# Performance work log

Hardware: AMD Instinct MI355X
Metric: run time of the kernel (lower is better)

## Reference

```python
import jax, jax.numpy as jnp
import numpy as np

EPS = 1e-5
NUM_GROUPS = 32


def group_norm(x, scale, bias):
    # x: [B, C, H, W], 32 groups, normalized over (C/G, H, W)
    B, C, H, W = x.shape
    G = NUM_GROUPS
    xg = x.reshape(B, G, C // G, H, W)
    mean = xg.mean(axis=(2, 3, 4), keepdims=True)
    var = xg.var(axis=(2, 3, 4), keepdims=True)
    xg = (xg - mean) * jax.lax.rsqrt(var + EPS)
    x = xg.reshape(B, C, H, W)
    return x * scale[None, :, None, None] + bias[None, :, None, None]


def setup_inputs() -> dict:
    key = jax.random.key(0)
    ks = jax.random.split(key, 6)
    B, C, H, W = 32, 512, 32, 32
    std = 1.0 / np.sqrt(C)
    return {
        "x": jax.random.normal(ks[0], (B, C, H, W), dtype=jnp.float32),
        "gn_scale": jnp.ones((C,), dtype=jnp.float32),
        "gn_bias": jnp.zeros((C,), dtype=jnp.float32),
        "wq": jax.random.normal(ks[1], (C, C), dtype=jnp.float32) * std,
        "bq": jnp.zeros((C,), dtype=jnp.float32),
        "wk": jax.random.normal(ks[2], (C, C), dtype=jnp.float32) * std,
        "bk": jnp.zeros((C,), dtype=jnp.float32),
        "wv": jax.random.normal(ks[3], (C, C), dtype=jnp.float32) * std,
        "bv": jnp.zeros((C,), dtype=jnp.float32),
        "wo": jax.random.normal(ks[4], (C, C), dtype=jnp.float32) * std,
        "bo": jnp.zeros((C,), dtype=jnp.float32),
    }


def reference(x, gn_scale, gn_bias, wq, bq, wk, bk, wv, bv, wo, bo):
    B, C, H, W = x.shape
    h = group_norm(x, gn_scale, gn_bias)
    # 1x1 convs == per-pixel matmuls; flatten spatial to tokens: [B, HW, C]
    ht = h.reshape(B, C, H * W).transpose(0, 2, 1)
    q = jnp.einsum('bnc,oc->bno', ht, wq) + bq  # [B, HW, C]
    k = jnp.einsum('bnc,oc->bno', ht, wk) + bk
    v = jnp.einsum('bnc,oc->bno', ht, wv) + bv
    scale = 1.0 / jnp.sqrt(jnp.asarray(C, x.dtype))
    w = jnp.einsum('bnc,bmc->bnm', q, k) * scale  # [B, HW, HW]
    w = jax.nn.softmax(w, axis=-1)
    a = jnp.einsum('bnm,bmc->bnc', w, v)  # [B, HW, C]
    out = jnp.einsum('bnc,oc->bno', a, wo) + bo
    out = out.transpose(0, 2, 1).reshape(B, C, H, W)
    return x + out
```

## Files before the change

kernel.cpp:

```cpp
#include <hip/hip_runtime.h>
#include <stdint.h>

typedef unsigned short u16;
typedef __attribute__((ext_vector_type(8))) short short8;
typedef __attribute__((ext_vector_type(4))) short s16x4;
typedef __attribute__((ext_vector_type(4))) float f32x4;

#define NTOK 1024
#define CDIM 512
#define NG 32

#define GLOAD_LDS16(gptr, lptr)                                                              \
  __builtin_amdgcn_global_load_lds((const __attribute__((address_space(1))) unsigned int*)(gptr), \
                                   (__attribute__((address_space(3))) unsigned int*)(lptr), 16, 0, 0)

__device__ __forceinline__ u16 f2bf(float f) {
  union { float f; uint32_t u; } v; v.f = f;
  uint32_t r = v.u + 0x7fffu + ((v.u >> 16) & 1u);
  return (u16)(r >> 16);
}

__device__ __forceinline__ float bf2f(u16 b) {
  union { uint32_t u; float f; } v; v.u = ((uint32_t)b) << 16;
  return v.f;
}

__global__ __launch_bounds__(256) void wconv(const float* __restrict__ wq, const float* __restrict__ wk,
                                             const float* __restrict__ wv, const float* __restrict__ wo,
                                             const float* __restrict__ bq, const float* __restrict__ bk,
                                             const float* __restrict__ bv,
                                             u16* __restrict__ out, float* __restrict__ bqkv) {
  int i = blockIdx.x * 256 + threadIdx.x;
  out[i]          = f2bf(wq[i]);
  out[262144 + i] = f2bf(wk[i]);
  out[524288 + i] = f2bf(wv[i]);
  out[786432 + i] = f2bf(wo[i]);
  if (i < 512) bqkv[i] = bq[i];
  else if (i < 1024) bqkv[i] = bk[i - 512];
  else if (i < 1536) bqkv[i] = bv[i - 1024];
}

__global__ __launch_bounds__(256) void gn_stats(const float* __restrict__ x,
                                                float* __restrict__ mean_o, float* __restrict__ rstd_o) {
  int bg = blockIdx.x;
  const float4* base = (const float4*)(x + (size_t)bg * 16384);
  float s = 0.f, ss = 0.f;
  for (int i = threadIdx.x; i < 4096; i += 256) {
    float4 v = base[i];
    s  += v.x + v.y + v.z + v.w;
    ss += v.x * v.x + v.y * v.y + v.z * v.z + v.w * v.w;
  }
#pragma unroll
  for (int d = 1; d < 64; d <<= 1) { s += __shfl_xor(s, d); ss += __shfl_xor(ss, d); }
  __shared__ float as[4], as2[4];
  int w = threadIdx.x >> 6;
  if ((threadIdx.x & 63) == 0) { as[w] = s; as2[w] = ss; }
  __syncthreads();
  if (threadIdx.x == 0) {
    float S = as[0] + as[1] + as[2] + as[3];
    float SS = as2[0] + as2[1] + as2[2] + as2[3];
    float m = S * (1.f / 16384.f);
    float var = SS * (1.f / 16384.f) - m * m;
    mean_o[bg] = m;
    rstd_o[bg] = rsqrtf(var + 1e-5f);
  }
}

__global__ __launch_bounds__(256) void gn_apply(const float* __restrict__ x,
                                                const float* __restrict__ mean_, const float* __restrict__ rstd_,
                                                const float* __restrict__ gsc, const float* __restrict__ gbi,
                                                u16* __restrict__ h) {
  int n0 = blockIdx.x * 64, c0 = blockIdx.y * 64, b = blockIdx.z;
  __shared__ u16 t[64][65];
  int tid = threadIdx.x;
  int nl4 = (tid & 15) * 4;
  int clb = tid >> 4;
#pragma unroll
  for (int p = 0; p < 4; ++p) {
    int cl = p * 16 + clb;
    int c = c0 + cl;
    int g = c >> 4;
    float m = mean_[b * NG + g], rs = rstd_[b * NG + g];
    float sc = gsc[c] * rs, bi = gbi[c] - m * sc;
    float4 v = *(const float4*)(x + ((size_t)b * CDIM + c) * NTOK + n0 + nl4);
    t[cl][nl4 + 0] = f2bf(v.x * sc + bi);
    t[cl][nl4 + 1] = f2bf(v.y * sc + bi);
    t[cl][nl4 + 2] = f2bf(v.z * sc + bi);
    t[cl][nl4 + 3] = f2bf(v.w * sc + bi);
  }
  __syncthreads();
  int nl = tid >> 3;
  int cc = (tid & 7) * 8;
#pragma unroll
  for (int p = 0; p < 2; ++p) {
    int n = nl + p * 32;
    short8 o;
#pragma unroll
    for (int i = 0; i < 8; ++i) o[i] = (short)t[cc + i][n];
    *(short8*)(h + (size_t)(b * NTOK + n0 + n) * CDIM + c0 + cc) = o;
  }
}

template <int MODE>
__device__ __forceinline__ void gemm_body(const u16* __restrict__ A, const u16* __restrict__ B,
                                          const float* __restrict__ bias, u16* __restrict__ outb,
                                          u16* __restrict__ outb2,
                                          float* __restrict__ outf, const float* __restrict__ resid,
                                          int Ka, int Kb, int nkt,
                                          size_t strideA, size_t strideB, int batch0) {
  int nx = gridDim.x, ny = gridDim.y;
  int nwg = nx * ny * gridDim.z;
  int id = blockIdx.x + nx * (blockIdx.y + ny * blockIdx.z);
  int cpx = nwg >> 3;
  int sw = (id & 7) * cpx + (id >> 3);
  int bx = sw % nx; int t_ = sw / nx;
  int by = t_ % ny; int z = t_ / ny;

  const u16* Amat = A + (size_t)z * strideA;
  const u16* Bmat = B + (size_t)z * strideB;
  int n0 = bx * 256, m0 = by * 256;
  __shared__ __align__(16) u16 SH[65536];
  int tid = threadIdx.x;
  int l = tid & 63, wid = tid >> 6;
  int lr = l & 15, lh = l >> 4;
  int wm = (wid >> 2) * 128;
  int wn = (wid & 3) * 64;

  f32x4 acc[8][4];
#pragma unroll
  for (int i = 0; i < 8; ++i)
#pragma unroll
    for (int j = 0; j < 4; ++j) acc[i][j] = (f32x4){0.f, 0.f, 0.f, 0.f};

  short8 af[4][2];
  short8 bf01[2][2];
  short8 bf23[2][2];

  int sr = tid >> 3, sc = tid & 7;
  int sg = (sc ^ (sr & 7)) << 3;
  const u16* Ag0 = Amat + (size_t)(m0 + sr) * Ka + sg;
  const u16* Ag1 = Ag0 + (size_t)64 * Ka;
  const u16* Bg0 = Bmat + (size_t)(n0 + sr) * Kb + sg;
  const u16* Bg1 = Bg0 + (size_t)64 * Kb;
  size_t hA = (size_t)128 * Ka, hB = (size_t)128 * Kb;
  u16* Al0 = SH + sr * 64 + sc * 8;
  u16* Bl0 = SH + 32768 + sr * 64 + sc * 8;

#define STAGE_A(bufsel, ktv, half)                                        \
  {                                                                       \
    size_t go_ = (size_t)(ktv) * 64 + ((half) ? hA : (size_t)0);          \
    u16* ld_ = Al0 + (bufsel) * 16384 + (half) * 8192;                    \
    GLOAD_LDS16(Ag0 + go_, ld_);                                          \
    GLOAD_LDS16(Ag1 + go_, ld_ + 4096);                                   \
  }
#define STAGE_B(bufsel, ktv, half)                                        \
  {                                                                       \
    size_t go_ = (size_t)(ktv) * 64 + ((half) ? hB : (size_t)0);          \
    u16* ld_ = Bl0 + (bufsel) * 16384 + (half) * 8192;                    \
    GLOAD_LDS16(Bg0 + go_, ld_);                                          \
    GLOAD_LDS16(Bg1 + go_, ld_ + 4096);                                   \
  }

#define READ_AF(ihalf, bufsel)                                                        \
  _Pragma("unroll") for (int i_ = 0; i_ < 4; ++i_) {                                  \
    int row_ = wm + (ihalf) * 64 + i_ * 16 + lr;                                      \
    const u16* p_ = SH + (bufsel) * 16384 + row_ * 64;                                \
    _Pragma("unroll") for (int ks_ = 0; ks_ < 2; ++ks_)                               \
      af[i_][ks_] = *(const short8*)(p_ + (((ks_ * 4 + lh) ^ (row_ & 7)) << 3));      \
  }

#define READ_BF(dst, jbase, bufsel)                                                   \
  _Pragma("unroll") for (int j_ = 0; j_ < 2; ++j_) {                                  \
    int row_ = wn + ((jbase) + j_) * 16 + lr;                                         \
    const u16* p_ = SH + 32768 + (bufsel) * 16384 + row_ * 64;                        \
    _Pragma("unroll") for (int ks_ = 0; ks_ < 2; ++ks_)                               \
      dst[j_][ks_] = *(const short8*)(p_ + (((ks_ * 4 + lh) ^ (row_ & 7)) << 3));     \
  }

#define MFMA_Q(ihalf, jbase, bsrc)                                                    \
  _Pragma("unroll") for (int ks_ = 0; ks_ < 2; ++ks_)                                 \
    _Pragma("unroll") for (int i_ = 0; i_ < 4; ++i_)                                  \
      _Pragma("unroll") for (int j_ = 0; j_ < 2; ++j_)                                \
        acc[(ihalf) * 4 + i_][(jbase) + j_] = __builtin_amdgcn_mfma_f32_16x16x32_bf16( \
            af[i_][ks_], bsrc[j_][ks_], acc[(ihalf) * 4 + i_][(jbase) + j_], 0, 0, 0);

#define PBAR() __builtin_amdgcn_s_barrier()

#define PHASES(BC, BN, GI, DOHI, DOLO)                                    \
  {                                                                       \
    int g1_ = (GI) + 1, g2_ = (GI) + 2;                                   \
                                           \
    READ_AF(0, BC);                                                       \
    READ_BF(bf01, 0, BC);                                                 \
    if (DOHI) { STAGE_A(BN, g1_, 1); }                                    \
    PBAR();                                                               \
    __builtin_amdgcn_s_setprio(1);                                        \
    MFMA_Q(0, 0, bf01);                                                   \
    __builtin_amdgcn_s_setprio(0);                                        \
    PBAR();                                                               \
                                           \
    READ_BF(bf23, 2, BC);                                                 \
    if (DOHI) { STAGE_B(BN, g1_, 1); }                                    \
    PBAR();                                                               \
    __builtin_amdgcn_s_setprio(1);                                        \
    MFMA_Q(0, 2, bf23);                                                   \
    __builtin_amdgcn_s_setprio(0);                                        \
    PBAR();                                                               \
     \
    READ_AF(1, BC);                                                       \
    if (DOLO) { STAGE_B(BC, g2_, 0); }                                    \
    PBAR();                                                               \
    __builtin_amdgcn_s_setprio(1);                                        \
    MFMA_Q(1, 2, bf23);                                                   \
    __builtin_amdgcn_s_setprio(0);                                        \
    PBAR();                                                               \
     \
    if (DOLO) { STAGE_A(BC, g2_, 0); }                                    \
    PBAR();                                                               \
    __builtin_amdgcn_s_setprio(1);                                        \
    MFMA_Q(1, 0, bf01);                                                   \
    __builtin_amdgcn_s_setprio(0);                                        \
    if (DOLO) { asm volatile("s_waitcnt vmcnt(4)"); }                     \
    else      { asm volatile("s_waitcnt vmcnt(0)"); }                     \
    __builtin_amdgcn_sched_barrier(0);                                    \
    PBAR();                                                               \
  }

  int k1 = (1 < nkt) ? 1 : 0;
  STAGE_B(0, 0, 0);
  STAGE_A(0, 0, 0);
  STAGE_A(0, 0, 1);
  STAGE_B(0, 0, 1);
  STAGE_B(1, k1, 0);
  STAGE_A(1, k1, 0);
  asm volatile("s_waitcnt vmcnt(4)");
  __builtin_amdgcn_sched_barrier(0);
  PBAR();

  for (int kt = 0; kt < nkt; kt += 2) {
    int more = (kt + 2 < nkt) ? 1 : 0;
    PHASES(0, 1, kt, 1, more);
    PHASES(1, 0, kt + 1, more, more);
  }

  __syncthreads();
  const int gr0 = m0 + wm, gc0 = n0 + wn;
  u16* eb = SH + wid * 4352;

  if constexpr (MODE == 5) {
    float bj[4];
#pragma unroll
    for (int j = 0; j < 4; ++j) bj[j] = bias[gc0 + j * 16 + lr];
    if (n0 < 1024) {
#pragma unroll
      for (int pass = 0; pass < 2; ++pass) {
#pragma unroll
        for (int i2 = 0; i2 < 4; ++i2)
#pragma unroll
          for (int j = 0; j < 4; ++j)
#pragma unroll
            for (int r = 0; r < 4; ++r)
              eb[(i2 * 16 + lh * 4 + r) * 68 + j * 16 + lr] =
                  f2bf(acc[pass * 4 + i2][j][r] + bj[j]);
        asm volatile("s_waitcnt lgkmcnt(0)");
        __builtin_amdgcn_sched_barrier(0);
#pragma unroll
        for (int t = 0; t < 8; ++t) {
          int row = t * 8 + (l >> 3), c8 = (l & 7) * 8;
          s16x4 lo = *(const s16x4*)(eb + row * 68 + c8);
          s16x4 hi = *(const s16x4*)(eb + row * 68 + c8 + 4);
          short8 o;
          o[0] = lo[0]; o[1] = lo[1]; o[2] = lo[2]; o[3] = lo[3];
          o[4] = hi[0]; o[5] = hi[1]; o[6] = hi[2]; o[7] = hi[3];
          *(short8*)(outb + (size_t)(gr0 + pass * 64 + row) * 1024 + gc0 + c8) = o;
        }
        asm volatile("s_waitcnt lgkmcnt(0)");
        __builtin_amdgcn_sched_barrier(0);
      }
    } else {
      int ch0 = gc0 - 1024;
      int bt = m0 >> 10, tok0 = (m0 & 1023) + wm;
#pragma unroll
      for (int pass = 0; pass < 2; ++pass) {
#pragma unroll
        for (int i2 = 0; i2 < 4; ++i2)
#pragma unroll
          for (int j = 0; j < 4; ++j) {
            s16x4 w;
#pragma unroll
            for (int r = 0; r < 4; ++r)
              w[r] = (short)f2bf(acc[pass * 4 + i2][j][r] + bj[j]);
            *(s16x4*)(eb + (j * 16 + lr) * 68 + i2 * 16 + lh * 4) = w;
          }
        asm volatile("s_waitcnt lgkmcnt(0)");
        __builtin_amdgcn_sched_barrier(0);
#pragma unroll
        for (int t = 0; t < 8; ++t) {
          int row = t * 8 + (l >> 3), c8 = (l & 7) * 8;
          s16x4 lo = *(const s16x4*)(eb + row * 68 + c8);
          s16x4 hi = *(const s16x4*)(eb + row * 68 + c8 + 4);
          short8 o;
          o[0] = lo[0]; o[1] = lo[1]; o[2] = lo[2]; o[3] = lo[3];
          o[4] = hi[0]; o[5] = hi[1]; o[6] = hi[2]; o[7] = hi[3];
          *(short8*)(outb2 + (size_t)(bt * 512 + ch0 + row) * 1024 + tok0 + pass * 64 + c8) = o;
        }
        asm volatile("s_waitcnt lgkmcnt(0)");
        __builtin_amdgcn_sched_barrier(0);
      }
    }
  } else if constexpr (MODE == 3 || MODE == 4) {
    u16* obase = (MODE == 3) ? (outb + (size_t)z * 1048576)
                             : (outb + (size_t)(batch0 + z) * 524288);
    const int LD = (MODE == 3) ? 1024 : 512;
#pragma unroll
    for (int pass = 0; pass < 2; ++pass) {
#pragma unroll
      for (int i2 = 0; i2 < 4; ++i2)
#pragma unroll
        for (int j = 0; j < 4; ++j)
#pragma unroll
          for (int r = 0; r < 4; ++r)
            eb[(i2 * 16 + lh * 4 + r) * 68 + j * 16 + lr] =
                f2bf(acc[pass * 4 + i2][j][r]);
      asm volatile("s_waitcnt lgkmcnt(0)");
      __builtin_amdgcn_sched_barrier(0);
#pragma unroll
      for (int t = 0; t < 8; ++t) {
        int row = t * 8 + (l >> 3), c8 = (l & 7) * 8;
        s16x4 lo = *(const s16x4*)(eb + row * 68 + c8);
        s16x4 hi = *(const s16x4*)(eb + row * 68 + c8 + 4);
        short8 o;
        o[0] = lo[0]; o[1] = lo[1]; o[2] = lo[2]; o[3] = lo[3];
        o[4] = hi[0]; o[5] = hi[1]; o[6] = hi[2]; o[7] = hi[3];
        *(short8*)(obase + (size_t)(gr0 + pass * 64 + row) * LD + gc0 + c8) = o;
      }
      asm volatile("s_waitcnt lgkmcnt(0)");
      __builtin_amdgcn_sched_barrier(0);
    }
  } else {
    float* ebf = (float*)SH + wid * 2176;
    int bt = n0 >> 10, nn0 = (n0 & 1023) + wn;
#pragma unroll
    for (int pass = 0; pass < 4; ++pass) {
#pragma unroll
      for (int i2 = 0; i2 < 2; ++i2)
#pragma unroll
        for (int r = 0; r < 4; ++r) {
          float bv = bias[gr0 + pass * 32 + i2 * 16 + lh * 4 + r];
#pragma unroll
          for (int j = 0; j < 4; ++j)
            ebf[(i2 * 16 + lh * 4 + r) * 68 + j * 16 + lr] =
                acc[pass * 2 + i2][j][r] + bv;
        }
      asm volatile("s_waitcnt lgkmcnt(0)");
      __builtin_amdgcn_sched_barrier(0);
#pragma unroll
      for (int t = 0; t < 8; ++t) {
        int row = t * 4 + (l >> 4), c4 = (l & 15) * 4;
        float4 vv = *(const float4*)(ebf + row * 68 + c4);
        size_t addr = ((size_t)bt * 512 + gr0 + pass * 32 + row) * 1024 + nn0 + c4;
        const float4 rr = *(const float4*)(resid + addr);
        vv.x += rr.x; vv.y += rr.y; vv.z += rr.z; vv.w += rr.w;
        *(float4*)(outf + addr) = vv;
      }
      asm volatile("s_waitcnt lgkmcnt(0)");
      __builtin_amdgcn_sched_barrier(0);
    }
  }
#undef STAGE_A
#undef STAGE_B
#undef READ_AF
#undef READ_BF
#undef MFMA_Q
#undef PBAR
#undef PHASES
}

__global__ __launch_bounds__(512, 2) void gemm_qkv(const u16* A, const u16* B, const float* bias,
                                                   u16* outb, u16* outb2, float* outf, const float* resid,
                                                   int Ka, int Kb, int nkt, size_t sA, size_t sB, int b0) {
  gemm_body<5>(A, B, bias, outb, outb2, outf, resid, Ka, Kb, nkt, sA, sB, b0);
}
__global__ __launch_bounds__(512, 2) void gemm_o(const u16* A, const u16* B, const float* bias,
                                                 u16* outb, u16* outb2, float* outf, const float* resid,
                                                 int Ka, int Kb, int nkt, size_t sA, size_t sB, int b0) {
  gemm_body<2>(A, B, bias, outb, outb2, outf, resid, Ka, Kb, nkt, sA, sB, b0);
}
__global__ __launch_bounds__(512, 2) void gemm_s(const u16* A, const u16* B, const float* bias,
                                                 u16* outb, u16* outb2, float* outf, const float* resid,
                                                 int Ka, int Kb, int nkt, size_t sA, size_t sB, int b0) {
  gemm_body<3>(A, B, bias, outb, outb2, outf, resid, Ka, Kb, nkt, sA, sB, b0);
}
__global__ __launch_bounds__(512, 2) void gemm_pv(const u16* A, const u16* B, const float* bias,
                                                  u16* outb, u16* outb2, float* outf, const float* resid,
                                                  int Ka, int Kb, int nkt, size_t sA, size_t sB, int b0) {
  gemm_body<4>(A, B, bias, outb, outb2, outf, resid, Ka, Kb, nkt, sA, sB, b0);
}

__global__ __launch_bounds__(256) void softmax_rows(u16* __restrict__ S) {
  const float scale = 0.04419417382415922f;
  int row = blockIdx.x * 4 + (threadIdx.x >> 6);
  int l = threadIdx.x & 63;
  u16* Sr = S + (size_t)row * 1024;
  short8 a = *(const short8*)(Sr + l * 8);
  short8 b = *(const short8*)(Sr + 512 + l * 8);
  float f[16];
#pragma unroll
  for (int i = 0; i < 8; ++i) { f[i] = bf2f((u16)a[i]); f[8 + i] = bf2f((u16)b[i]); }
  float mx = f[0];
#pragma unroll
  for (int i = 1; i < 16; ++i) mx = fmaxf(mx, f[i]);
#pragma unroll
  for (int d = 1; d < 64; d <<= 1) mx = fmaxf(mx, __shfl_xor(mx, d));
  float s = 0.f;
#pragma unroll
  for (int i = 0; i < 16; ++i) { f[i] = __expf((f[i] - mx) * scale); s += f[i]; }
#pragma unroll
  for (int d = 1; d < 64; d <<= 1) s += __shfl_xor(s, d);
  float inv = 1.f / s;
  short8 oa, ob;
#pragma unroll
  for (int i = 0; i < 8; ++i) { oa[i] = (short)f2bf(f[i] * inv); ob[i] = (short)f2bf(f[8 + i] * inv); }
  *(short8*)(Sr + l * 8) = oa;
  *(short8*)(Sr + 512 + l * 8) = ob;
}

extern "C" void kernel_launch(void* const* d_in, const int* in_sizes, int n_in,
                              void* d_out, int out_size, void* d_ws, size_t ws_size,
                              hipStream_t stream) {
  const float* x   = (const float*)d_in[0];
  const float* gsc = (const float*)d_in[1];
  const float* gbi = (const float*)d_in[2];
  const float* wq  = (const float*)d_in[3];
  const float* bq  = (const float*)d_in[4];
  const float* wk  = (const float*)d_in[5];
  const float* bk  = (const float*)d_in[6];
  const float* wv  = (const float*)d_in[7];
  const float* bv  = (const float*)d_in[8];
  const float* wo  = (const float*)d_in[9];
  const float* bo  = (const float*)d_in[10];

  char* ws = (char*)d_ws;
  u16* wbf = (u16*)ws;
  float* bqkv = (float*)(ws + (2ull << 20));
  float* mean_ = (float*)(ws + (2ull << 20) + 65536);
  float* rstd_ = mean_ + 1024;
  u16* h   = (u16*)(ws + (4ull << 20));
  u16* qk  = (u16*)(ws + (36ull << 20));
  u16* vm  = (u16*)(ws + (100ull << 20));
  u16* S   = (u16*)(ws + (132ull << 20));
  u16* am  = h;
  float* out = (float*)d_out;

  size_t sbytes = ws_size > (132ull << 20) ? ws_size - (132ull << 20) : 0;
  int CB = 1;
  while (CB < 32 && (size_t)(CB * 2) * (2ull << 20) <= sbytes) CB *= 2;

  wconv<<<1024, 256, 0, stream>>>(wq, wk, wv, wo, bq, bk, bv, wbf, bqkv);
  gn_stats<<<1024, 256, 0, stream>>>(x, mean_, rstd_);
  gn_apply<<<dim3(16, 8, 32), 256, 0, stream>>>(x, mean_, rstd_, gsc, gbi, h);
  gemm_qkv<<<dim3(6, 128), 512, 0, stream>>>(h, wbf, bqkv, qk, vm, nullptr, nullptr,
                                             512, 512, 8, 0, 0, 0);
  for (int c0 = 0; c0 < 32; c0 += CB) {
    gemm_s<<<dim3(4, 4, CB), 512, 0, stream>>>(qk + (size_t)c0 * 1048576, qk + 512 + (size_t)c0 * 1048576,
                                               nullptr, S, nullptr, nullptr, nullptr,
                                               1024, 1024, 8, 1048576, 1048576, 0);
    softmax_rows<<<CB * 256, 256, 0, stream>>>(S);
    gemm_pv<<<dim3(2, 4, CB), 512, 0, stream>>>(S, vm + (size_t)c0 * 524288,
                                                nullptr, am, nullptr, nullptr, nullptr,
                                                1024, 1024, 16, 1048576, 524288, c0);
  }
  gemm_o<<<dim3(128, 2), 512, 0, stream>>>(wbf + 786432, am, bo, nullptr, nullptr, out, x,
                                           512, 512, 8, 0, 0, 0);
}
```

Before: 241.8 us.

## Fuse softmax into score GEMM epilogue and PV GEMM row-sum normalization

Drops the separate softmax kernel. The score GEMM epilogue now writes exp(score*scale) directly in bf16. The PV GEMM sums each row of its A fragments (the exp values) while loading them, reduces those sums across lanes, keeps them in LDS, and divides the output rows by them in a new MODE 4 epilogue. This removes a full read and write pass over the 1024x1024 score matrix per batch. The cost is extra ALU work inside the PV main loop, and dropping the max-subtraction step risks overflow if scores grow large.

```diff
diff --git a/kernel.cpp b/kernel.cpp
--- a/kernel.cpp
+++ b/kernel.cpp
@@ -132,6 +132,10 @@
 #pragma unroll
     for (int j = 0; j < 4; ++j) acc[i][j] = (f32x4){0.f, 0.f, 0.f, 0.f};
 
+  float rs[8];
+#pragma unroll
+  for (int i = 0; i < 8; ++i) rs[i] = 0.f;
+
   short8 af[4][2];
   short8 bf01[2][2];
   short8 bf23[2][2];
@@ -169,6 +173,14 @@
       af[i_][ks_] = *(const short8*)(p_ + (((ks_ * 4 + lh) ^ (row_ & 7)) << 3));      \
   }
 
+#define SUM_AF(ihalf)                                                                 \
+  if (MODE == 4) {                                                                    \
+    _Pragma("unroll") for (int i_ = 0; i_ < 4; ++i_)                                  \
+      _Pragma("unroll") for (int ks_ = 0; ks_ < 2; ++ks_)                             \
+        _Pragma("unroll") for (int e_ = 0; e_ < 8; ++e_)                              \
+          rs[(ihalf) * 4 + i_] += bf2f((u16)af[i_][ks_][e_]);                         \
+  }
+
 #define READ_BF(dst, jbase, bufsel)                                                   \
   _Pragma("unroll") for (int j_ = 0; j_ < 2; ++j_) {                                  \
     int row_ = wn + ((jbase) + j_) * 16 + lr;                                         \
@@ -191,6 +203,7 @@
     int g1_ = (GI) + 1, g2_ = (GI) + 2;                                   \
                                            \
     READ_AF(0, BC);                                                       \
+    SUM_AF(0);                                                            \
     READ_BF(bf01, 0, BC);                                                 \
     if (DOHI) { STAGE_A(BN, g1_, 1); }                                    \
     PBAR();                                                               \
@@ -208,6 +221,7 @@
     PBAR();                                                               \
      \
     READ_AF(1, BC);                                                       \
+    SUM_AF(1);                                                            \
     if (DOLO) { STAGE_B(BC, g2_, 0); }                                    \
     PBAR();                                                               \
     __builtin_amdgcn_s_setprio(1);                                        \
@@ -241,6 +255,20 @@
     int more = (kt + 2 < nkt) ? 1 : 0;
     PHASES(0, 1, kt, 1, more);
     PHASES(1, 0, kt + 1, more, more);
+  }
+
+  if (MODE == 4) {
+#pragma unroll
+    for (int p = 0; p < 8; ++p) {
+      rs[p] += __shfl_xor(rs[p], 16);
+      rs[p] += __shfl_xor(rs[p], 32);
+    }
+    if (lh == 0) {
+      float* rsum_ = (float*)(SH + 64512);
+#pragma unroll
+      for (int p = 0; p < 8; ++p)
+        rsum_[wm + (p >> 2) * 64 + (p & 3) * 16 + lr] = rs[p];
+    }
   }
 
   __syncthreads();
@@ -308,10 +336,9 @@
         __builtin_amdgcn_sched_barrier(0);
       }
     }
-  } else if constexpr (MODE == 3 || MODE == 4) {
-    u16* obase = (MODE == 3) ? (outb + (size_t)z * 1048576)
-                             : (outb + (size_t)(batch0 + z) * 524288);
-    const int LD = (MODE == 3) ? 1024 : 512;
+  } else if constexpr (MODE == 3) {
+    const float scale = 0.04419417382415922f;
+    u16* obase = outb + (size_t)z * 1048576;
 #pragma unroll
     for (int pass = 0; pass < 2; ++pass) {
 #pragma unroll
@@ -321,7 +348,7 @@
 #pragma unroll
           for (int r = 0; r < 4; ++r)
             eb[(i2 * 16 + lh * 4 + r) * 68 + j * 16 + lr] =
-                f2bf(acc[pass * 4 + i2][j][r]);
+                f2bf(__expf(acc[pass * 4 + i2][j][r] * scale));
       asm volatile("s_waitcnt lgkmcnt(0)");
       __builtin_amdgcn_sched_barrier(0);
 #pragma unroll
@@ -332,7 +359,37 @@
         short8 o;
         o[0] = lo[0]; o[1] = lo[1]; o[2] = lo[2]; o[3] = lo[3];
         o[4] = hi[0]; o[5] = hi[1]; o[6] = hi[2]; o[7] = hi[3];
-        *(short8*)(obase + (size_t)(gr0 + pass * 64 + row) * LD + gc0 + c8) = o;
+        *(short8*)(obase + (size_t)(gr0 + pass * 64 + row) * 1024 + gc0 + c8) = o;
+      }
+      asm volatile("s_waitcnt lgkmcnt(0)");
+      __builtin_amdgcn_sched_barrier(0);
+    }
+  } else if constexpr (MODE == 4) {
+    const float* rsum_ = (const float*)(SH + 64512);
+    u16* obase = outb + (size_t)(batch0 + z) * 524288;
+#pragma unroll
+    for (int pass = 0; pass < 2; ++pass) {
+#pragma unroll
+      for (int i2 = 0; i2 < 4; ++i2)
+#pragma unroll
+        for (int r = 0; r < 4; ++r) {
+          float inv_ = 1.f / rsum_[wm + pass * 64 + i2 * 16 + lh * 4 + r];
+#pragma unroll
+          for (int j = 0; j < 4; ++j)
+            eb[(i2 * 16 + lh * 4 + r) * 68 + j * 16 + lr] =
+                f2bf(acc[pass * 4 + i2][j][r] * inv_);
+        }
+      asm volatile("s_waitcnt lgkmcnt(0)");
+      __builtin_amdgcn_sched_barrier(0);
+#pragma unroll
+      for (int t = 0; t < 8; ++t) {
+        int row = t * 8 + (l >> 3), c8 = (l & 7) * 8;
+        s16x4 lo = *(const s16x4*)(eb + row * 68 + c8);
+        s16x4 hi = *(const s16x4*)(eb + row * 68 + c8 + 4);
+        short8 o;
+        o[0] = lo[0]; o[1] = lo[1]; o[2] = lo[2]; o[3] = lo[3];
+        o[4] = hi[0]; o[5] = hi[1]; o[6] = hi[2]; o[7] = hi[3];
+        *(short8*)(obase + (size_t)(gr0 + pass * 64 + row) * 512 + gc0 + c8) = o;
       }
       asm volatile("s_waitcnt lgkmcnt(0)");
       __builtin_amdgcn_sched_barrier(0);
@@ -370,6 +427,7 @@
 #undef STAGE_A
 #undef STAGE_B
 #undef READ_AF
+#undef SUM_AF
 #undef READ_BF
 #undef MFMA_Q
 #undef PBAR
@@ -395,34 +453,6 @@
                                                   u16* outb, u16* outb2, float* outf, const float* resid,
                                                   int Ka, int Kb, int nkt, size_t sA, size_t sB, int b0) {
   gemm_body<4>(A, B, bias, outb, outb2, outf, resid, Ka, Kb, nkt, sA, sB, b0);
-}
-
-__global__ __launch_bounds__(256) void softmax_rows(u16* __restrict__ S) {
-  const float scale = 0.04419417382415922f;
-  int row = blockIdx.x * 4 + (threadIdx.x >> 6);
-  int l = threadIdx.x & 63;
-  u16* Sr = S + (size_t)row * 1024;
-  short8 a = *(const short8*)(Sr + l * 8);
-  short8 b = *(const short8*)(Sr + 512 + l * 8);
-  float f[16];
-#pragma unroll
-  for (int i = 0; i < 8; ++i) { f[i] = bf2f((u16)a[i]); f[8 + i] = bf2f((u16)b[i]); }
-  float mx = f[0];
-#pragma unroll
-  for (int i = 1; i < 16; ++i) mx = fmaxf(mx, f[i]);
-#pragma unroll
-  for (int d = 1; d < 64; d <<= 1) mx = fmaxf(mx, __shfl_xor(mx, d));
-  float s = 0.f;
-#pragma unroll
-  for (int i = 0; i < 16; ++i) { f[i] = __expf((f[i] - mx) * scale); s += f[i]; }
-#pragma unroll
-  for (int d = 1; d < 64; d <<= 1) s += __shfl_xor(s, d);
-  float inv = 1.f / s;
-  short8 oa, ob;
-#pragma unroll
-  for (int i = 0; i < 8; ++i) { oa[i] = (short)f2bf(f[i] * inv); ob[i] = (short)f2bf(f[8 + i] * inv); }
-  *(short8*)(Sr + l * 8) = oa;
-  *(short8*)(Sr + 512 + l * 8) = ob;
 }
 
 extern "C" void kernel_launch(void* const* d_in, const int* in_sizes, int n_in,
@@ -465,7 +495,6 @@
     gemm_s<<<dim3(4, 4, CB), 512, 0, stream>>>(qk + (size_t)c0 * 1048576, qk + 512 + (size_t)c0 * 1048576,
                                                nullptr, S, nullptr, nullptr, nullptr,
                                                1024, 1024, 8, 1048576, 1048576, 0);
-    softmax_rows<<<CB * 256, 256, 0, stream>>>(S);
     gemm_pv<<<dim3(2, 4, CB), 512, 0, stream>>>(S, vm + (size_t)c0 * 524288,
                                                 nullptr, am, nullptr, nullptr, nullptr,
                                                 1024, 1024, 16, 1048576, 524288, c0);
```

Result: slower. 384.2 us (+58.9%).
